# Kernel tuning notes

Measured on AMD Instinct MI355X. Metric: run time of the kernel, lower is better.

## Reference

```python
import jax, jax.numpy as jnp
import numpy as np

B, T, C = 4, 2048, 1024
H, HS = 16, 64


def setup_inputs() -> dict:
    key = jax.random.key(0)
    ks = jax.random.split(key, 5)
    scale = (H * C) ** (-0.5)
    x = jax.random.normal(ks[0], (B, T, C), dtype=jnp.float32)
    Wk = jax.random.normal(ks[1], (H, C, HS), dtype=jnp.float32) * scale
    Wq = jax.random.normal(ks[2], (H, C, HS), dtype=jnp.float32) * scale
    Wv = jax.random.normal(ks[3], (H, C, HS), dtype=jnp.float32) * scale
    proj_w = jax.random.normal(ks[4], (C, C), dtype=jnp.float32) / C ** 0.5
    proj_b = jnp.zeros((C,), dtype=jnp.float32)
    return {"x": x, "Wk": Wk, "Wq": Wq, "Wv": Wv, "proj_w": proj_w, "proj_b": proj_b}


def reference(x, Wk, Wq, Wv, proj_w, proj_b):
    b, t, c = x.shape
    # per-head projections: (B,T,C) x (H,C,D) -> (B,H,T,D)
    q = jnp.einsum('btc,hcd->bhtd', x, Wq)
    k = jnp.einsum('btc,hcd->bhtd', x, Wk)
    v = jnp.einsum('btc,hcd->bhtd', x, Wv)
    # NOTE: original module does not scale by 1/sqrt(head_size)
    wei = jnp.einsum('bhtd,bhsd->bhts', q, k)  # (B,H,T,T)
    causal = jnp.tril(jnp.ones((t, t), dtype=bool))
    wei = jnp.where(causal, wei, -jnp.inf)
    wei = jax.nn.softmax(wei, axis=-1)
    out = jnp.einsum('bhts,bhsd->bhtd', wei, v)
    out = out.transpose(0, 2, 1, 3).reshape(b, t, c)  # concat heads
    return out @ proj_w + proj_b
```

## Files before the change

### kernel.cpp

```cpp
#include <hip/hip_runtime.h>

typedef unsigned short u16;
typedef u16 u16x4 __attribute__((ext_vector_type(4)));
typedef u16 u16x8 __attribute__((ext_vector_type(8)));
typedef unsigned uint2v __attribute__((ext_vector_type(2)));
typedef unsigned uint4v __attribute__((ext_vector_type(4)));
typedef __bf16 bf16x2 __attribute__((ext_vector_type(2)));
typedef __bf16 bf16x8 __attribute__((ext_vector_type(8)));
typedef float f32x4 __attribute__((ext_vector_type(4)));

#define DEV static __device__ __forceinline__

DEV u16 f2bf(float f) {
  union { float f; unsigned u; } v; v.f = f;
  return (u16)((v.u + 0x7FFFu + ((v.u >> 16) & 1u)) >> 16);
}

DEV void async16(const void* g, void* l) {
  __builtin_amdgcn_global_load_lds((const __attribute__((address_space(1))) void*)g,
                                   (__attribute__((address_space(3))) void*)l, 16, 0, 0);
}

DEV f32x4 mfma16(bf16x8 a, bf16x8 b, f32x4 c) {
  return __builtin_amdgcn_mfma_f32_16x16x32_bf16(a, b, c, 0, 0, 0);
}

DEV float exp2fast(float x) { return __builtin_amdgcn_exp2f(x); }

#define BARRIER() asm volatile("s_barrier" ::: "memory")
#define SB0() __builtin_amdgcn_sched_barrier(0)

__global__ __launch_bounds__(256) void k_prep(const float* __restrict__ x,
                                              const float* __restrict__ Wk,
                                              const float* __restrict__ Wq,
                                              const float* __restrict__ Wv,
                                              const float* __restrict__ pw,
                                              u16* __restrict__ xb,
                                              u16* __restrict__ wT,
                                              u16* __restrict__ pwT) {
  __shared__ float t[64 * 72];
  const int bid = blockIdx.x, tid = threadIdx.x;
  if (bid < 8192) {
    int i = bid * 1024 + tid * 4;
    float4 v = *(const float4*)(x + i);
    u16x4 o = { f2bf(v.x), f2bf(v.y), f2bf(v.z), f2bf(v.w) };
    *(u16x4*)(xb + i) = o;
    return;
  }
  const int role = bid - 8192;
  const float* src;
  u16* dst;
  int rows, cols, bx, by, bz;
  float scale;
  if (role < 768) {
    const int w = role >> 8, rem = role & 255;
    src = (w == 0) ? Wq : ((w == 1) ? Wk : Wv);
    dst = wT + (size_t)w * 1024 * 1024;
    scale = (w == 0) ? 1.44269504088896340736f : 1.0f;
    rows = 1024; cols = 64; bx = 0; by = rem >> 4; bz = rem & 15;
  } else {
    const int p = role - 768;
    src = pw; dst = pwT; scale = 1.0f;
    rows = 1024; cols = 1024; bx = p & 15; by = p >> 4; bz = 0;
  }
  src += (size_t)bz * rows * cols;
  dst += (size_t)bz * rows * cols;
  const int c0 = bx * 64, r0 = by * 64;
  const int rr = tid >> 2, cb = (tid & 3) * 16;
  const float* s = src + (size_t)(r0 + rr) * cols + c0 + cb;
  float4 v0 = *(const float4*)(s + 0);
  float4 v1 = *(const float4*)(s + 4);
  float4 v2 = *(const float4*)(s + 8);
  float4 v3 = *(const float4*)(s + 12);
  *(float4*)(t + rr * 72 + cb + 0)  = v0;
  *(float4*)(t + rr * 72 + cb + 4)  = v1;
  *(float4*)(t + rr * 72 + cb + 8)  = v2;
  *(float4*)(t + rr * 72 + cb + 12) = v3;
  __syncthreads();
  const int dd = tid >> 2, eb = (tid & 3) * 16;
  u16x8 o0, o1;
#pragma unroll
  for (int e = 0; e < 8; ++e) o0[e] = f2bf(t[(eb + e) * 72 + dd] * scale);
#pragma unroll
  for (int e = 0; e < 8; ++e) o1[e] = f2bf(t[(eb + 8 + e) * 72 + dd] * scale);
  u16* dp = dst + (size_t)(c0 + dd) * rows + r0 + eb;
  *(u16x8*)dp = o0;
  *(u16x8*)(dp + 8) = o1;
}

template <int MODE>
__global__ __launch_bounds__(512, 2) void k_gemm(const u16* __restrict__ A,
                                                 const u16* __restrict__ Bt,
                                                 u16* __restrict__ qd,
                                                 u16* __restrict__ kd,
                                                 u16* __restrict__ vd,
                                                 float* __restrict__ out,
                                                 const float* __restrict__ bias) {
  constexpr int BN   = (MODE == 0) ? 192 : 128;
  constexpr int AI   = (MODE == 0) ? 8 : 4;
  constexpr int AJ   = (MODE == 0) ? 3 : 4;
  constexpr int GB   = BN / 64;
  constexpr int GXC  = (MODE == 0) ? 16 : 8;
  constexpr int SLOT = (256 + BN) * 64;
  constexpr int RING = (MODE == 0) ? 2 : 3;
  __shared__ u16 lds[RING * SLOT];

  const int tid = threadIdx.x;
  const int w = tid >> 6, lane = tid & 63;
  const int quad = lane >> 4, l15 = lane & 15;
  const int wm = (MODE == 0) ? (w >> 2) : (w >> 1);
  const int wn = (MODE == 0) ? (w & 3) : (w & 1);

  constexpr int NWG = GXC * 32;
  int lin = (int)blockIdx.y * GXC + (int)blockIdx.x;
  lin = (lin & 7) * (NWG >> 3) + (lin >> 3);
  const size_t mb = (size_t)(lin / GXC);
  const int nb = lin % GXC;

  const int lr = lane >> 3;
  const int lc = ((lane & 7) ^ lr) << 3;
  const u16* ga0 = A  + (mb * 256 + (size_t)(w * 8 + lr)) * 1024 + lc;
  const u16* gb0 = Bt + ((size_t)nb * BN + (size_t)(w * 8 + lr)) * 1024 + lc;

  const int swz0 = ((0 + quad) ^ (l15 & 7)) << 3;
  const int swz1 = ((4 + quad) ^ (l15 & 7)) << 3;

  f32x4 acc[AI][AJ] = {};

  if constexpr (MODE == 0) {
    {
      u16* sb = lds + w * 512;
#pragma unroll
      for (int g = 0; g < 4; ++g) async16(ga0 + (size_t)g * 65536, sb + g * 4096);
#pragma unroll
      for (int g = 0; g < GB; ++g) async16(gb0 + (size_t)g * 65536, sb + 16384 + g * 4096);
    }
    asm volatile("s_waitcnt vmcnt(0)" ::: "memory");
    BARRIER(); SB0();

    for (int s = 0; s < 16; ++s) {
      const u16* Ab = lds + (s & 1) * SLOT;
      const u16* Bb = Ab + 16384;
      u16* nsb = lds + ((s + 1) & 1) * SLOT + w * 512;
      const int ko = (s + 1) * 64;

      bf16x8 a0[AI], b0[AJ];
#pragma unroll
      for (int i = 0; i < AI; ++i)
        a0[i] = *(const bf16x8*)(Ab + (wm * (AI * 16) + i * 16 + l15) * 64 + swz0);
#pragma unroll
      for (int j = 0; j < AJ; ++j)
        b0[j] = *(const bf16x8*)(Bb + (wn * (AJ * 16) + j * 16 + l15) * 64 + swz0);
      if (s < 15) {
#pragma unroll
        for (int g = 0; g < 4; ++g)
          async16(ga0 + (size_t)g * 65536 + ko, nsb + g * 4096);
      }
      SB0(); BARRIER(); SB0();
      __builtin_amdgcn_s_setprio(1);
#pragma unroll
      for (int i = 0; i < AI; ++i)
#pragma unroll
        for (int j = 0; j < AJ; ++j) acc[i][j] = mfma16(a0[i], b0[j], acc[i][j]);
      __builtin_amdgcn_s_setprio(0);
      SB0(); BARRIER(); SB0();

      bf16x8 a1[AI], b1[AJ];
#pragma unroll
      for (int i = 0; i < AI; ++i)
        a1[i] = *(const bf16x8*)(Ab + (wm * (AI * 16) + i * 16 + l15) * 64 + swz1);
#pragma unroll
      for (int j = 0; j < AJ; ++j)
        b1[j] = *(const bf16x8*)(Bb + (wn * (AJ * 16) + j * 16 + l15) * 64 + swz1);
      if (s < 15) {
#pragma unroll
        for (int g = 0; g < GB; ++g)
          async16(gb0 + (size_t)g * 65536 + ko, nsb + 16384 + g * 4096);
      }
      SB0(); BARRIER(); SB0();
      __builtin_amdgcn_s_setprio(1);
#pragma unroll
      for (int i = 0; i < AI; ++i)
#pragma unroll
        for (int j = 0; j < AJ; ++j) acc[i][j] = mfma16(a1[i], b1[j], acc[i][j]);
      __builtin_amdgcn_s_setprio(0);
      SB0();
      if (s < 15) {
        asm volatile("s_waitcnt vmcnt(0) lgkmcnt(0)" ::: "memory");
        BARRIER(); SB0();
      }
    }
  } else {
    auto STAGE = [&](int buf, int s) {
      u16* sb = lds + buf * SLOT + w * 512;
      const int ko = s * 64;
#pragma unroll
      for (int g = 0; g < 4; ++g)
        async16(ga0 + (size_t)g * 65536 + ko, sb + g * 4096);
#pragma unroll
      for (int g = 0; g < GB; ++g)
        async16(gb0 + (size_t)g * 65536 + ko, sb + 16384 + g * 4096);
    };
    STAGE(0, 0);
    STAGE(1, 1);
    asm volatile("s_waitcnt vmcnt(6)" ::: "memory");
    BARRIER(); SB0();

    for (int s = 0; s < 16; ++s) {
      const u16* Ab = lds + (s % 3) * SLOT;
      const u16* Bb = Ab + 16384;

      bf16x8 a0[AI], b0[AJ];
#pragma unroll
      for (int i = 0; i < AI; ++i)
        a0[i] = *(const bf16x8*)(Ab + (wm * (AI * 16) + i * 16 + l15) * 64 + swz0);
#pragma unroll
      for (int j = 0; j < AJ; ++j)
        b0[j] = *(const bf16x8*)(Bb + (wn * (AJ * 16) + j * 16 + l15) * 64 + swz0);
      if (s < 14) {
        u16* d = lds + ((s + 2) % 3) * SLOT + w * 512;
        async16(ga0 + 0 * 65536 + (s + 2) * 64, d + 0 * 4096);
        async16(ga0 + 1 * 65536 + (s + 2) * 64, d + 1 * 4096);
        async16(ga0 + 2 * 65536 + (s + 2) * 64, d + 2 * 4096);
      }
      SB0(); BARRIER(); SB0();
      __builtin_amdgcn_s_setprio(1);
#pragma unroll
      for (int i = 0; i < AI; ++i)
#pragma unroll
        for (int j = 0; j < AJ; ++j) acc[i][j] = mfma16(a0[i], b0[j], acc[i][j]);
      __builtin_amdgcn_s_setprio(0);
      SB0(); BARRIER(); SB0();

      bf16x8 a1[AI], b1[AJ];
#pragma unroll
      for (int i = 0; i < AI; ++i)
        a1[i] = *(const bf16x8*)(Ab + (wm * (AI * 16) + i * 16 + l15) * 64 + swz1);
#pragma unroll
      for (int j = 0; j < AJ; ++j)
        b1[j] = *(const bf16x8*)(Bb + (wn * (AJ * 16) + j * 16 + l15) * 64 + swz1);
      if (s < 14) {
        u16* d = lds + ((s + 2) % 3) * SLOT + w * 512;
        async16(ga0 + 3 * 65536 + (s + 2) * 64, d + 3 * 4096);
        async16(gb0 + 0 * 65536 + (s + 2) * 64, d + 16384 + 0 * 4096);
        async16(gb0 + 1 * 65536 + (s + 2) * 64, d + 16384 + 4096);
      }
      SB0(); BARRIER(); SB0();
      __builtin_amdgcn_s_setprio(1);
#pragma unroll
      for (int i = 0; i < AI; ++i)
#pragma unroll
        for (int j = 0; j < AJ; ++j) acc[i][j] = mfma16(a1[i], b1[j], acc[i][j]);
      __builtin_amdgcn_s_setprio(0);
      SB0();
      if (s < 14)       { asm volatile("s_waitcnt vmcnt(6)" ::: "memory"); }
      else if (s == 14) { asm volatile("s_waitcnt vmcnt(0)" ::: "memory"); }
      if (s < 15) { BARRIER(); SB0(); }
    }
  }

  const size_t m0 = mb * 256 + wm * (AI * 16);
  const int n0 = nb * BN + wn * (AJ * 16);
  if (MODE == 0) {
#pragma unroll
    for (int j = 0; j < AJ; ++j) {
      const int n = n0 + j * 16 + l15;
      const int p = n >> 10, hh = (n >> 6) & 15, d = n & 63;
      if (p == 2) {
#pragma unroll
        for (int i = 0; i < AI; ++i) {
          const size_t m = m0 + i * 16 + quad * 4;
          const size_t bb = m >> 11, tt = m & 2047;
          u16x4 pk = { f2bf(acc[i][j][0]), f2bf(acc[i][j][1]),
                       f2bf(acc[i][j][2]), f2bf(acc[i][j][3]) };
          *(u16x4*)(vd + ((bb * 16 + hh) * 64 + d) * 2048 + tt) = pk;
        }
      } else {
        u16* dst = (p == 0) ? qd : kd;
#pragma unroll
        for (int i = 0; i < AI; ++i)
#pragma unroll
          for (int r = 0; r < 4; ++r) {
            const size_t m = m0 + i * 16 + quad * 4 + r;
            const size_t bb = m >> 11, tt = m & 2047;
            dst[((bb * 16 + hh) * 2048 + tt) * 64 + d] = f2bf(acc[i][j][r]);
          }
      }
    }
  } else {
#pragma unroll
    for (int j = 0; j < AJ; ++j) {
      const int n = n0 + j * 16 + l15;
      const float bv = bias[n];
#pragma unroll
      for (int i = 0; i < AI; ++i)
#pragma unroll
        for (int r = 0; r < 4; ++r) {
          const size_t m = m0 + i * 16 + quad * 4 + r;
          out[m * 1024 + n] = acc[i][j][r] + bv;
        }
    }
  }
}

__global__ __launch_bounds__(512) void k_attn(const u16* __restrict__ Qg,
                                              const u16* __restrict__ Kg,
                                              const u16* __restrict__ Vtg,
                                              u16* __restrict__ Og) {
  __shared__ u16 Kbuf[2 * 4096];
  __shared__ u16 Vbuf[2 * 4096];
  const int tid = threadIdx.x;
  const int wave = tid >> 6, lane = tid & 63;
  const int quad = lane >> 4, l15 = lane & 15;
  const int quad4 = quad * 4, quad8 = quad * 8;
  const int bh = blockIdx.x;
  const int qb = 7 - (int)blockIdx.y;
  const u16* kg = Kg + (size_t)bh * 2048 * 64;
  const u16* vg = Vtg + (size_t)bh * 64 * 2048;
  const int b = bh >> 4, h = bh & 15;

  const int lrow = lane >> 3;
  const int lchunk = ((lane & 7) ^ lrow) << 3;
  const u16* kst = kg + (size_t)(wave * 8 + lrow) * 64 + lchunk;
  const u16* vst = vg + (size_t)(wave * 8 + lrow) * 2048 + lchunk;
  u16* kdst0 = Kbuf + wave * 512;
  u16* vdst0 = Vbuf + wave * 512;

  const int rowoff = l15 * 64;
  const int swz0 = ((0 + quad) ^ (l15 & 7)) << 3;
  const int swz1 = ((4 + quad) ^ (l15 & 7)) << 3;

  const int qlo = qb * 256 + wave * 32;
  const int ntw = 4 * qb + 1 + (wave >> 1);
  const int ntb = 4 * qb + 4;
  const u16* qg = Qg + ((size_t)bh * 2048 + (size_t)qb * 256) * 64;

  bf16x8 qf[2][2];
#pragma unroll
  for (int i = 0; i < 2; ++i)
#pragma unroll
    for (int c = 0; c < 2; ++c)
      qf[i][c] = *(const bf16x8*)(qg + (size_t)(wave * 32 + i * 16 + l15) * 64 +
                                  c * 32 + quad8);

  f32x4 oacc[2][4] = {};
  f32x4 lacc[2] = {};
  const f32x4 fzero = {};
  const u16x8 onesu = {0x3F80, 0x3F80, 0x3F80, 0x3F80,
                       0x3F80, 0x3F80, 0x3F80, 0x3F80};
  const bf16x8 onesf = __builtin_bit_cast(bf16x8, onesu);

  async16(kst, kdst0);
  async16(vst, vdst0);

  for (int it = 0; it < ntb; ++it) {
    __syncthreads();

    if (it + 1 < ntb) {
      const int buf = (it + 1) & 1;
      const size_t s0n = (size_t)(it + 1) * 64;
      async16(kst + s0n * 64, kdst0 + buf * 4096);
      async16(vst + s0n,      vdst0 + buf * 4096);
    }

    if (it < ntw) {
      const int s0 = it * 64;
      const u16* Kb = Kbuf + (it & 1) * 4096;
      const u16* Vb = Vbuf + (it & 1) * 4096;

      f32x4 sacc[4][2];
      __builtin_amdgcn_s_setprio(1);
#pragma unroll
      for (int j = 0; j < 4; ++j) {
        bf16x8 kf0 = *(const bf16x8*)(Kb + j * 1024 + rowoff + swz0);
        bf16x8 kf1 = *(const bf16x8*)(Kb + j * 1024 + rowoff + swz1);
        sacc[j][0] = mfma16(kf0, qf[0][0], fzero);
        sacc[j][0] = mfma16(kf1, qf[0][1], sacc[j][0]);
        sacc[j][1] = mfma16(kf0, qf[1][0], fzero);
        sacc[j][1] = mfma16(kf1, qf[1][1], sacc[j][1]);
      }
      __builtin_amdgcn_s_setprio(0);

#pragma unroll
      for (int j = 0; j < 4; ++j)
#pragma unroll
        for (int i = 0; i < 2; ++i)
#pragma unroll
          for (int r = 0; r < 4; ++r)
            sacc[j][i][r] = exp2fast(sacc[j][i][r]);

      if (it == ntw - 1) {
#pragma unroll
        for (int j = 0; j < 4; ++j)
#pragma unroll
        for (int i = 0; i < 2; ++i)
#pragma unroll
          for (int r = 0; r < 4; ++r)
            if (s0 + j * 16 + quad4 + r > qlo + i * 16 + l15) sacc[j][i][r] = 0.f;
      }

      bf16x8 pa[2][2];
#pragma unroll
      for (int i = 0; i < 2; ++i) {
        unsigned P[8];
#pragma unroll
        for (int j = 0; j < 4; ++j) {
          bf16x2 lo = { (__bf16)sacc[j][i][0], (__bf16)sacc[j][i][1] };
          bf16x2 hi = { (__bf16)sacc[j][i][2], (__bf16)sacc[j][i][3] };
          P[j * 2 + 0] = __builtin_bit_cast(unsigned, lo);
          P[j * 2 + 1] = __builtin_bit_cast(unsigned, hi);
        }
        unsigned wd[8];
#pragma unroll
        for (int g = 0; g < 4; ++g) {
          const int x = (g & 2) * 2 + (g & 1);
          uint2v t = __builtin_amdgcn_permlane32_swap(P[x], P[x + 2], false, false);
          uint2v u = __builtin_amdgcn_permlane16_swap(t.x, t.y, false, false);
          wd[x] = u.x;
          wd[x + 2] = u.y;
        }
        uint4v lo4 = { wd[0], wd[1], wd[2], wd[3] };
        uint4v hi4 = { wd[4], wd[5], wd[6], wd[7] };
        pa[i][0] = __builtin_bit_cast(bf16x8, lo4);
        pa[i][1] = __builtin_bit_cast(bf16x8, hi4);
      }

      __builtin_amdgcn_s_setprio(1);
#pragma unroll
      for (int n = 0; n < 4; ++n) {
        bf16x8 vf0 = *(const bf16x8*)(Vb + n * 1024 + rowoff + swz0);
        bf16x8 vf1 = *(const bf16x8*)(Vb + n * 1024 + rowoff + swz1);
        oacc[0][n] = mfma16(pa[0][0], vf0, oacc[0][n]);
        oacc[0][n] = mfma16(pa[0][1], vf1, oacc[0][n]);
        oacc[1][n] = mfma16(pa[1][0], vf0, oacc[1][n]);
        oacc[1][n] = mfma16(pa[1][1], vf1, oacc[1][n]);
      }
      lacc[0] = mfma16(pa[0][0], onesf, lacc[0]);
      lacc[0] = mfma16(pa[0][1], onesf, lacc[0]);
      lacc[1] = mfma16(pa[1][0], onesf, lacc[1]);
      lacc[1] = mfma16(pa[1][1], onesf, lacc[1]);
      __builtin_amdgcn_s_setprio(0);
    }
  }

#pragma unroll
  for (int i = 0; i < 2; ++i)
#pragma unroll
    for (int r = 0; r < 4; ++r) {
      const float inv = 1.0f / lacc[i][r];
      const size_t t = (size_t)qb * 256 + wave * 32 + i * 16 + quad4 + r;
#pragma unroll
      for (int n = 0; n < 4; ++n)
        Og[((size_t)b * 2048 + t) * 1024 + h * 64 + n * 16 + l15] =
            f2bf(oacc[i][n][r] * inv);
    }
}

extern "C" void kernel_launch(void* const* d_in, const int* in_sizes, int n_in,
                              void* d_out, int out_size, void* d_ws, size_t ws_size,
                              hipStream_t stream) {
  const float* x  = (const float*)d_in[0];
  const float* Wk = (const float*)d_in[1];
  const float* Wq = (const float*)d_in[2];
  const float* Wv = (const float*)d_in[3];
  const float* pw = (const float*)d_in[4];
  const float* pb = (const float*)d_in[5];
  float* out = (float*)d_out;
  char* ws = (char*)d_ws;

  u16* xb  = (u16*)(ws + 0);
  u16* wT  = (u16*)(ws + 16777216);
  u16* pwT = (u16*)(ws + 23068672);
  u16* q   = (u16*)(ws + 25165824);
  u16* kb  = (u16*)(ws + 41943040);
  u16* vt  = (u16*)(ws + 58720256);
  u16* att = (u16*)(ws + 0);

  k_prep<<<9216, 256, 0, stream>>>(x, Wk, Wq, Wv, pw, xb, wT, pwT);
  k_gemm<0><<<dim3(16, 32), 512, 0, stream>>>(xb, wT, q, kb, vt, nullptr, nullptr);
  k_attn<<<dim3(64, 8), 512, 0, stream>>>(q, kb, vt, att);
  k_gemm<1><<<dim3(8, 32), 512, 0, stream>>>(att, pwT, nullptr, nullptr, nullptr, out, pb);
}
```

Baseline: 229.4 us.

## Widen QKV GEMM tile to 256x256 and split K-step into row-half phases

The QKV projection GEMM tile grows from 256x192 to 256x256 (AJ 4, 12 column blocks), cutting the grid from 512 to 384 workgroups and raising MFMA work per LDS load. The K-step is reorganised so each phase computes half the A rows over the full K=64 slice. Global-to-LDS loads are split into two interleaved chunks guarded by partial vmcnt waits rather than a full drain. The cost is more LDS and registers per workgroup and fewer workgroups, which may hurt occupancy and the tail wave.

```diff
diff --git a/kernel.cpp b/kernel.cpp
--- a/kernel.cpp
+++ b/kernel.cpp
@@ -96,11 +96,11 @@
                                                  u16* __restrict__ vd,
                                                  float* __restrict__ out,
                                                  const float* __restrict__ bias) {
-  constexpr int BN   = (MODE == 0) ? 192 : 128;
+  constexpr int BN   = (MODE == 0) ? 256 : 128;
   constexpr int AI   = (MODE == 0) ? 8 : 4;
-  constexpr int AJ   = (MODE == 0) ? 3 : 4;
+  constexpr int AJ   = 4;
   constexpr int GB   = BN / 64;
-  constexpr int GXC  = (MODE == 0) ? 16 : 8;
+  constexpr int GXC  = (MODE == 0) ? 12 : 8;
   constexpr int SLOT = (256 + BN) * 64;
   constexpr int RING = (MODE == 0) ? 2 : 3;
   __shared__ u16 lds[RING * SLOT];
@@ -128,65 +128,70 @@
   f32x4 acc[AI][AJ] = {};
 
   if constexpr (MODE == 0) {
-    {
-      u16* sb = lds + w * 512;
-#pragma unroll
-      for (int g = 0; g < 4; ++g) async16(ga0 + (size_t)g * 65536, sb + g * 4096);
-#pragma unroll
-      for (int g = 0; g < GB; ++g) async16(gb0 + (size_t)g * 65536, sb + 16384 + g * 4096);
-    }
+    auto stA = [&](int p, int c, int ko) {
+      async16(ga0 + (size_t)c * 65536 + ko, lds + p * SLOT + c * 4096 + w * 512);
+    };
+    auto stB = [&](int p, int c, int ko) {
+      async16(gb0 + (size_t)c * 65536 + ko,
+              lds + p * SLOT + 16384 + c * 4096 + w * 512);
+    };
+    stA(0, 0, 0); stA(0, 2, 0); stB(0, 0, 0); stB(0, 1, 0);
+    stB(0, 2, 0); stB(0, 3, 0); stA(0, 1, 0); stA(0, 3, 0);
     asm volatile("s_waitcnt vmcnt(0)" ::: "memory");
     BARRIER(); SB0();
 
     for (int s = 0; s < 16; ++s) {
-      const u16* Ab = lds + (s & 1) * SLOT;
+      const int r = s & 1, p = r ^ 1;
+      const int ko = (s + 1) * 64;
+      const u16* Ab = lds + r * SLOT;
       const u16* Bb = Ab + 16384;
-      u16* nsb = lds + ((s + 1) & 1) * SLOT + w * 512;
-      const int ko = (s + 1) * 64;
-
-      bf16x8 a0[AI], b0[AJ];
-#pragma unroll
-      for (int i = 0; i < AI; ++i)
-        a0[i] = *(const bf16x8*)(Ab + (wm * (AI * 16) + i * 16 + l15) * 64 + swz0);
-#pragma unroll
-      for (int j = 0; j < AJ; ++j)
-        b0[j] = *(const bf16x8*)(Bb + (wn * (AJ * 16) + j * 16 + l15) * 64 + swz0);
-      if (s < 15) {
-#pragma unroll
-        for (int g = 0; g < 4; ++g)
-          async16(ga0 + (size_t)g * 65536 + ko, nsb + g * 4096);
-      }
+
+      bf16x8 b0[4], b1[4], a0[4], a1[4];
+#pragma unroll
+      for (int j = 0; j < 4; ++j) {
+        b0[j] = *(const bf16x8*)(Bb + (wn * 64 + j * 16 + l15) * 64 + swz0);
+        b1[j] = *(const bf16x8*)(Bb + (wn * 64 + j * 16 + l15) * 64 + swz1);
+      }
+#pragma unroll
+      for (int i = 0; i < 4; ++i) {
+        a0[i] = *(const bf16x8*)(Ab + (wm * 128 + i * 16 + l15) * 64 + swz0);
+        a1[i] = *(const bf16x8*)(Ab + (wm * 128 + i * 16 + l15) * 64 + swz1);
+      }
+      if (s < 15) { stA(p, 0, ko); stA(p, 2, ko); stB(p, 0, ko); stB(p, 1, ko); }
       SB0(); BARRIER(); SB0();
       __builtin_amdgcn_s_setprio(1);
 #pragma unroll
-      for (int i = 0; i < AI; ++i)
-#pragma unroll
-        for (int j = 0; j < AJ; ++j) acc[i][j] = mfma16(a0[i], b0[j], acc[i][j]);
-      __builtin_amdgcn_s_setprio(0);
+      for (int i = 0; i < 4; ++i)
+#pragma unroll
+        for (int j = 0; j < 4; ++j) {
+          acc[i][j] = mfma16(a0[i], b0[j], acc[i][j]);
+          acc[i][j] = mfma16(a1[i], b1[j], acc[i][j]);
+        }
+      __builtin_amdgcn_s_setprio(0);
+      SB0();
+      if (s < 15) { asm volatile("s_waitcnt vmcnt(4)" ::: "memory"); }
+      else        { asm volatile("s_waitcnt vmcnt(0)" ::: "memory"); }
+      BARRIER(); SB0();
+
+#pragma unroll
+      for (int i = 0; i < 4; ++i) {
+        a0[i] = *(const bf16x8*)(Ab + (wm * 128 + (i + 4) * 16 + l15) * 64 + swz0);
+        a1[i] = *(const bf16x8*)(Ab + (wm * 128 + (i + 4) * 16 + l15) * 64 + swz1);
+      }
+      if (s < 15) { stB(p, 2, ko); stB(p, 3, ko); stA(p, 1, ko); stA(p, 3, ko); }
       SB0(); BARRIER(); SB0();
-
-      bf16x8 a1[AI], b1[AJ];
-#pragma unroll
-      for (int i = 0; i < AI; ++i)
-        a1[i] = *(const bf16x8*)(Ab + (wm * (AI * 16) + i * 16 + l15) * 64 + swz1);
-#pragma unroll
-      for (int j = 0; j < AJ; ++j)
-        b1[j] = *(const bf16x8*)(Bb + (wn * (AJ * 16) + j * 16 + l15) * 64 + swz1);
-      if (s < 15) {
-#pragma unroll
-        for (int g = 0; g < GB; ++g)
-          async16(gb0 + (size_t)g * 65536 + ko, nsb + 16384 + g * 4096);
-      }
-      SB0(); BARRIER(); SB0();
-      __builtin_amdgcn_s_setprio(1);
-#pragma unroll
-      for (int i = 0; i < AI; ++i)
-#pragma unroll
-        for (int j = 0; j < AJ; ++j) acc[i][j] = mfma16(a1[i], b1[j], acc[i][j]);
+      __builtin_amdgcn_s_setprio(1);
+#pragma unroll
+      for (int i = 0; i < 4; ++i)
+#pragma unroll
+        for (int j = 0; j < 4; ++j) {
+          acc[i + 4][j] = mfma16(a0[i], b0[j], acc[i + 4][j]);
+          acc[i + 4][j] = mfma16(a1[i], b1[j], acc[i + 4][j]);
+        }
       __builtin_amdgcn_s_setprio(0);
       SB0();
       if (s < 15) {
-        asm volatile("s_waitcnt vmcnt(0) lgkmcnt(0)" ::: "memory");
+        asm volatile("s_waitcnt vmcnt(2) lgkmcnt(0)" ::: "memory");
         BARRIER(); SB0();
       }
     }
@@ -477,7 +482,7 @@
   u16* att = (u16*)(ws + 0);
 
   k_prep<<<9216, 256, 0, stream>>>(x, Wk, Wq, Wv, pw, xb, wT, pwT);
-  k_gemm<0><<<dim3(16, 32), 512, 0, stream>>>(xb, wT, q, kb, vt, nullptr, nullptr);
+  k_gemm<0><<<dim3(12, 32), 512, 0, stream>>>(xb, wT, q, kb, vt, nullptr, nullptr);
   k_attn<<<dim3(64, 8), 512, 0, stream>>>(q, kb, vt, att);
   k_gemm<1><<<dim3(8, 32), 512, 0, stream>>>(att, pwT, nullptr, nullptr, nullptr, out, pb);
 }
```

Result: slower. 238.1 us (+3.8%).

## Software-pipeline attention loop: overlap QK^T of next tile with softmax/PV of previous

Applied to the files above, without the earlier changes.

Restructures the attention main loop so each step issues the QK^T MFMAs for tile it while finishing exp, masking, permlane packing and PV MFMAs for tile it-1. The score accumulators ping-pong between two register sets, and V moves to a triple-buffered LDS ring so the in-flight tile is not overwritten. The intent is to hide softmax VALU latency behind matrix-core work. The cost is extra VGPR pressure from the second score set, which could cut occupancy, and 8KB more LDS.

```diff
diff --git a/kernel.cpp b/kernel.cpp
--- a/kernel.cpp
+++ b/kernel.cpp
@@ -308,7 +308,7 @@
                                               const u16* __restrict__ Vtg,
                                               u16* __restrict__ Og) {
   __shared__ u16 Kbuf[2 * 4096];
-  __shared__ u16 Vbuf[2 * 4096];
+  __shared__ u16 Vbuf[3 * 4096];
   const int tid = threadIdx.x;
   const int wave = tid >> 6, lane = tid & 63;
   const int quad = lane >> 4, l15 = lane & 15;
@@ -350,98 +350,101 @@
                        0x3F80, 0x3F80, 0x3F80, 0x3F80};
   const bf16x8 onesf = __builtin_bit_cast(bf16x8, onesu);
 
-  async16(kst, kdst0);
-  async16(vst, vdst0);
-
-  for (int it = 0; it < ntb; ++it) {
-    __syncthreads();
-
+  auto finish = [&](int tt, f32x4 (&S)[4][2]) {
+    const int s0 = tt * 64;
+#pragma unroll
+    for (int j = 0; j < 4; ++j)
+#pragma unroll
+      for (int i = 0; i < 2; ++i)
+#pragma unroll
+        for (int r = 0; r < 4; ++r)
+          S[j][i][r] = exp2fast(S[j][i][r]);
+    if (tt == ntw - 1) {
+#pragma unroll
+      for (int j = 0; j < 4; ++j)
+#pragma unroll
+      for (int i = 0; i < 2; ++i)
+#pragma unroll
+        for (int r = 0; r < 4; ++r)
+          if (s0 + j * 16 + quad4 + r > qlo + i * 16 + l15) S[j][i][r] = 0.f;
+    }
+    bf16x8 pa[2][2];
+#pragma unroll
+    for (int i = 0; i < 2; ++i) {
+      unsigned P[8];
+#pragma unroll
+      for (int j = 0; j < 4; ++j) {
+        bf16x2 lo = { (__bf16)S[j][i][0], (__bf16)S[j][i][1] };
+        bf16x2 hi = { (__bf16)S[j][i][2], (__bf16)S[j][i][3] };
+        P[j * 2 + 0] = __builtin_bit_cast(unsigned, lo);
+        P[j * 2 + 1] = __builtin_bit_cast(unsigned, hi);
+      }
+      unsigned wd[8];
+#pragma unroll
+      for (int g = 0; g < 4; ++g) {
+        const int x = (g & 2) * 2 + (g & 1);
+        uint2v t = __builtin_amdgcn_permlane32_swap(P[x], P[x + 2], false, false);
+        uint2v u = __builtin_amdgcn_permlane16_swap(t.x, t.y, false, false);
+        wd[x] = u.x;
+        wd[x + 2] = u.y;
+      }
+      uint4v lo4 = { wd[0], wd[1], wd[2], wd[3] };
+      uint4v hi4 = { wd[4], wd[5], wd[6], wd[7] };
+      pa[i][0] = __builtin_bit_cast(bf16x8, lo4);
+      pa[i][1] = __builtin_bit_cast(bf16x8, hi4);
+    }
+    const u16* Vb = Vbuf + (tt % 3) * 4096;
+    __builtin_amdgcn_s_setprio(1);
+#pragma unroll
+    for (int n = 0; n < 4; ++n) {
+      bf16x8 vf0 = *(const bf16x8*)(Vb + n * 1024 + rowoff + swz0);
+      bf16x8 vf1 = *(const bf16x8*)(Vb + n * 1024 + rowoff + swz1);
+      oacc[0][n] = mfma16(pa[0][0], vf0, oacc[0][n]);
+      oacc[0][n] = mfma16(pa[0][1], vf1, oacc[0][n]);
+      oacc[1][n] = mfma16(pa[1][0], vf0, oacc[1][n]);
+      oacc[1][n] = mfma16(pa[1][1], vf1, oacc[1][n]);
+    }
+    lacc[0] = mfma16(pa[0][0], onesf, lacc[0]);
+    lacc[0] = mfma16(pa[0][1], onesf, lacc[0]);
+    lacc[1] = mfma16(pa[1][0], onesf, lacc[1]);
+    lacc[1] = mfma16(pa[1][1], onesf, lacc[1]);
+    __builtin_amdgcn_s_setprio(0);
+  };
+
+  auto step = [&](int it, f32x4 (&CUR)[4][2], f32x4 (&PRV)[4][2]) {
     if (it + 1 < ntb) {
-      const int buf = (it + 1) & 1;
       const size_t s0n = (size_t)(it + 1) * 64;
-      async16(kst + s0n * 64, kdst0 + buf * 4096);
-      async16(vst + s0n,      vdst0 + buf * 4096);
-    }
-
+      async16(kst + s0n * 64, kdst0 + ((it + 1) & 1) * 4096);
+      async16(vst + s0n,      vdst0 + ((it + 1) % 3) * 4096);
+    }
     if (it < ntw) {
-      const int s0 = it * 64;
       const u16* Kb = Kbuf + (it & 1) * 4096;
-      const u16* Vb = Vbuf + (it & 1) * 4096;
-
-      f32x4 sacc[4][2];
       __builtin_amdgcn_s_setprio(1);
 #pragma unroll
       for (int j = 0; j < 4; ++j) {
         bf16x8 kf0 = *(const bf16x8*)(Kb + j * 1024 + rowoff + swz0);
         bf16x8 kf1 = *(const bf16x8*)(Kb + j * 1024 + rowoff + swz1);
-        sacc[j][0] = mfma16(kf0, qf[0][0], fzero);
-        sacc[j][0] = mfma16(kf1, qf[0][1], sacc[j][0]);
-        sacc[j][1] = mfma16(kf0, qf[1][0], fzero);
-        sacc[j][1] = mfma16(kf1, qf[1][1], sacc[j][1]);
+        CUR[j][0] = mfma16(kf0, qf[0][0], fzero);
+        CUR[j][0] = mfma16(kf1, qf[0][1], CUR[j][0]);
+        CUR[j][1] = mfma16(kf0, qf[1][0], fzero);
+        CUR[j][1] = mfma16(kf1, qf[1][1], CUR[j][1]);
       }
       __builtin_amdgcn_s_setprio(0);
-
-#pragma unroll
-      for (int j = 0; j < 4; ++j)
-#pragma unroll
-        for (int i = 0; i < 2; ++i)
-#pragma unroll
-          for (int r = 0; r < 4; ++r)
-            sacc[j][i][r] = exp2fast(sacc[j][i][r]);
-
-      if (it == ntw - 1) {
-#pragma unroll
-        for (int j = 0; j < 4; ++j)
-#pragma unroll
-        for (int i = 0; i < 2; ++i)
-#pragma unroll
-          for (int r = 0; r < 4; ++r)
-            if (s0 + j * 16 + quad4 + r > qlo + i * 16 + l15) sacc[j][i][r] = 0.f;
-      }
-
-      bf16x8 pa[2][2];
-#pragma unroll
-      for (int i = 0; i < 2; ++i) {
-        unsigned P[8];
-#pragma unroll
-        for (int j = 0; j < 4; ++j) {
-          bf16x2 lo = { (__bf16)sacc[j][i][0], (__bf16)sacc[j][i][1] };
-          bf16x2 hi = { (__bf16)sacc[j][i][2], (__bf16)sacc[j][i][3] };
-          P[j * 2 + 0] = __builtin_bit_cast(unsigned, lo);
-          P[j * 2 + 1] = __builtin_bit_cast(unsigned, hi);
-        }
-        unsigned wd[8];
-#pragma unroll
-        for (int g = 0; g < 4; ++g) {
-          const int x = (g & 2) * 2 + (g & 1);
-          uint2v t = __builtin_amdgcn_permlane32_swap(P[x], P[x + 2], false, false);
-          uint2v u = __builtin_amdgcn_permlane16_swap(t.x, t.y, false, false);
-          wd[x] = u.x;
-          wd[x + 2] = u.y;
-        }
-        uint4v lo4 = { wd[0], wd[1], wd[2], wd[3] };
-        uint4v hi4 = { wd[4], wd[5], wd[6], wd[7] };
-        pa[i][0] = __builtin_bit_cast(bf16x8, lo4);
-        pa[i][1] = __builtin_bit_cast(bf16x8, hi4);
-      }
-
-      __builtin_amdgcn_s_setprio(1);
-#pragma unroll
-      for (int n = 0; n < 4; ++n) {
-        bf16x8 vf0 = *(const bf16x8*)(Vb + n * 1024 + rowoff + swz0);
-        bf16x8 vf1 = *(const bf16x8*)(Vb + n * 1024 + rowoff + swz1);
-        oacc[0][n] = mfma16(pa[0][0], vf0, oacc[0][n]);
-        oacc[0][n] = mfma16(pa[0][1], vf1, oacc[0][n]);
-        oacc[1][n] = mfma16(pa[1][0], vf0, oacc[1][n]);
-        oacc[1][n] = mfma16(pa[1][1], vf1, oacc[1][n]);
-      }
-      lacc[0] = mfma16(pa[0][0], onesf, lacc[0]);
-      lacc[0] = mfma16(pa[0][1], onesf, lacc[0]);
-      lacc[1] = mfma16(pa[1][0], onesf, lacc[1]);
-      lacc[1] = mfma16(pa[1][1], onesf, lacc[1]);
-      __builtin_amdgcn_s_setprio(0);
-    }
+    }
+    if (it > 0 && it - 1 < ntw) finish(it - 1, PRV);
+    __syncthreads();
+  };
+
+  async16(kst, kdst0);
+  async16(vst, vdst0);
+  __syncthreads();
+
+  f32x4 sA[4][2], sB[4][2];
+  for (int ii = 0; ii < ntb; ii += 2) {
+    step(ii + 0, sA, sB);
+    step(ii + 1, sB, sA);
   }
+  if (ntb - 1 < ntw) finish(ntb - 1, sB);
 
 #pragma unroll
   for (int i = 0; i < 2; ++i)
```

Measured after the change: 228.5 us. About the same (-0.4%).
